# Kernel optimization log

Hardware: AMD Instinct MI355X
Metric: run time of the kernel (lower is better)

The kernel has to match this reference:

```python
import jax, jax.numpy as jnp
import numpy as np

B, S, D, H = 2, 2048, 1024, 16
HD = D // H


def setup_inputs() -> dict:
    key = jax.random.key(0)
    ks = jax.random.split(key, 12)
    s = 1.0 / np.sqrt(D)
    inp = {
        "queries": jax.random.normal(ks[0], (B, S, D), jnp.float32),
        "keys": jax.random.normal(ks[1], (B, S, D), jnp.float32),
        "values": jax.random.normal(ks[2], (B, S, D), jnp.float32),
        # True = masked out (causal upper triangle)
        "attn_mask": jnp.triu(jnp.ones((S, S), bool), k=1),
        "W_q": jax.random.normal(ks[3], (D, D), jnp.float32) * s,
        "b_q": jnp.zeros((D,), jnp.float32),
        "W_k": jax.random.normal(ks[4], (D, D), jnp.float32) * s,
        "b_k": jnp.zeros((D,), jnp.float32),
        "W_v": jax.random.normal(ks[5], (D, D), jnp.float32) * s,
        "b_v": jnp.zeros((D,), jnp.float32),
        "W_o": jax.random.normal(ks[6], (D, D), jnp.float32) * s,
        "b_o": jnp.zeros((D,), jnp.float32),
    }
    return inp


def _split_heads(x):
    b, s, _ = x.shape
    return x.reshape(b, s, H, HD).transpose(0, 2, 1, 3)  # (B,H,S,HD)


def reference(queries, keys, values, attn_mask, W_q, b_q, W_k, b_k, W_v, b_v, W_o, b_o):
    Q = _split_heads(queries @ W_q + b_q)
    K = _split_heads(keys @ W_k + b_k)
    V = _split_heads(values @ W_v + b_v)
    scale = 1.0 / np.sqrt(HD)
    scores = jnp.einsum("bhqd,bhkd->bhqk", Q, K) * scale  # (B,H,S,S)
    scores = jnp.where(attn_mask, jnp.float32(-1e9), scores)
    probs = jax.nn.softmax(scores, axis=-1)
    ctx = jnp.einsum("bhqk,bhkd->bhqd", probs, V)
    ctx = ctx.transpose(0, 2, 1, 3).reshape(queries.shape[0], queries.shape[1], D)
    return ctx @ W_o + b_o
```

## Files before the change

### kernel.cpp

```cpp
#include <hip/hip_runtime.h>
#include <hip/hip_bf16.h>
#include <math.h>

typedef __bf16 bf16x8 __attribute__((ext_vector_type(8)));
typedef float f32x4 __attribute__((ext_vector_type(4)));
typedef unsigned short u16x8 __attribute__((ext_vector_type(8)));
typedef unsigned short u16x4 __attribute__((ext_vector_type(4)));

static __device__ __forceinline__ unsigned short f2bf(float f) {
    union { float f; unsigned u; } v; v.f = f;
    unsigned r = v.u + 0x7fffu + ((v.u >> 16) & 1u);
    return (unsigned short)(r >> 16);
}

static __device__ __forceinline__ float exp2fast(float x) {
    return __builtin_exp2f(x);
}

static __device__ __forceinline__ void gload16(const void* g, void* l) {
    __builtin_amdgcn_global_load_lds((const __attribute__((address_space(1))) unsigned int*)g,
                                     (__attribute__((address_space(3))) unsigned int*)l, 16, 0, 0);
}

#define MFMA16(a, b, c) __builtin_amdgcn_mfma_f32_16x16x32_bf16((a), (b), (c), 0, 0, 0)

static __device__ __forceinline__ bf16x8 frag_swz(const unsigned short* base, int row, int chunk) {
    return *(const bf16x8*)((const char*)base + row * 128 + (((chunk ^ row) & 7) << 4));
}

struct PrepArgs {
    const float* act[3]; unsigned short* actout[3];
    const float* W[4];   unsigned short* Wt[4];
};

__global__ void prep_kernel(PrepArgs a) {
    __shared__ __align__(16) unsigned short Ws[64][66];
    const int b = blockIdx.x, t = threadIdx.x;
    if (b < 6144) {
        const int sel = b >> 11;
        const size_t i = (((size_t)(b & 2047)) * 256 + t) * 8;
        const float* in = a.act[sel];
        f32x4 v0 = *(const f32x4*)(in + i);
        f32x4 v1 = *(const f32x4*)(in + i + 4);
        u16x8 o;
#pragma unroll
        for (int j = 0; j < 4; ++j) { o[j] = f2bf(v0[j]); o[j + 4] = f2bf(v1[j]); }
        *(u16x8*)(a.actout[sel] + i) = o;
        return;
    }
    const int idx = b - 6144;
    const int z = idx >> 8;
    const int rem = idx & 255;
    const int c0 = (rem & 15) * 64;
    const int r0 = (rem >> 4) * 64;
    const float* W = a.W[z];
    unsigned short* Wt = a.Wt[z];
#pragma unroll
    for (int p = 0; p < 4; ++p) {
        int lin = p * 256 + t;
        int r = lin >> 4, cc = (lin & 15) * 4;
        f32x4 v = *(const f32x4*)(W + (size_t)(r0 + r) * 1024 + c0 + cc);
#pragma unroll
        for (int j = 0; j < 4; ++j) Ws[r][cc + j] = f2bf(v[j]);
    }
    __syncthreads();
#pragma unroll
    for (int p = 0; p < 2; ++p) {
        int lin = p * 256 + t;
        int n = lin >> 3, kc = (lin & 7) * 8;
        u16x8 o;
#pragma unroll
        for (int j = 0; j < 8; ++j) o[j] = Ws[kc + j][n];
        *(u16x8*)(Wt + (size_t)(c0 + n) * 1024 + r0 + kc) = o;
    }
}

struct QkvArgs {
    const unsigned short* A[3];
    const unsigned short* Wt[3];
    const float* bias[3];
    unsigned short* out[3];
    float scale[3];
};

__global__ __launch_bounds__(256, 3)
void gemm_qkv(QkvArgs p)
{
    __shared__ __align__(16) unsigned short As[128 * 64];
    __shared__ __align__(16) unsigned short Bs[128 * 64];

    const int z = blockIdx.z;
    const unsigned short* A  = p.A[z];
    const unsigned short* Bt = p.Wt[z];
    const float* bias = p.bias[z];
    unsigned short* out = p.out[z];
    const float oscale = p.scale[z];

    const int t = threadIdx.x, lane = t & 63, w = t >> 6;
    const int lr = lane & 15, lh = lane >> 4;
    const int m0 = blockIdx.y * 128, n0 = blockIdx.x * 128;
    const int wm = (w >> 1) * 64, wn = (w & 1) * 64;
    const int wbase = (t & 0xC0) * 8;

    f32x4 acc[4][4];
#pragma unroll
    for (int i = 0; i < 4; ++i)
#pragma unroll
        for (int j = 0; j < 4; ++j)
#pragma unroll
            for (int e = 0; e < 4; ++e) acc[i][j][e] = 0.0f;

    for (int kt = 0; kt < 16; ++kt) {
        const int k0 = kt << 6;
        __syncthreads();
#pragma unroll
        for (int q = 0; q < 4; ++q) {
            int lin = q * 256 + t;
            int row = lin >> 3, sc = (lin ^ (lin >> 3)) & 7;
            gload16(A + (size_t)(m0 + row) * 1024 + k0 + sc * 8, &As[q * 2048 + wbase]);
        }
#pragma unroll
        for (int q = 0; q < 4; ++q) {
            int lin = q * 256 + t;
            int row = lin >> 3, sc = (lin ^ (lin >> 3)) & 7;
            gload16(Bt + (size_t)(n0 + row) * 1024 + k0 + sc * 8, &Bs[q * 2048 + wbase]);
        }
        __syncthreads();
#pragma unroll
        for (int kb = 0; kb < 2; ++kb) {
            bf16x8 a[4], b[4];
#pragma unroll
            for (int i = 0; i < 4; ++i) a[i] = frag_swz(As, wm + i * 16 + lr, kb * 4 + lh);
#pragma unroll
            for (int j = 0; j < 4; ++j) b[j] = frag_swz(Bs, wn + j * 16 + lr, kb * 4 + lh);
#pragma unroll
            for (int i = 0; i < 4; ++i)
#pragma unroll
                for (int j = 0; j < 4; ++j)
                    acc[i][j] = MFMA16(a[i], b[j], acc[i][j]);
        }
    }

#pragma unroll
    for (int i = 0; i < 4; ++i) {
#pragma unroll
        for (int j = 0; j < 4; ++j) {
            const int gcol = n0 + wn + j * 16 + lr;
            const float bv = bias[gcol];
            const int h_ = gcol >> 6, hd_ = gcol & 63;
            if (z == 2) {
                const int grow0 = m0 + wm + i * 16 + lh * 4;
                const int b_ = grow0 >> 11, s_ = grow0 & 2047;
                u16x4 pk;
#pragma unroll
                for (int r = 0; r < 4; ++r) pk[r] = f2bf((acc[i][j][r] + bv) * oscale);
                *(u16x4*)(out + (((size_t)((b_ * 16 + h_) * 64 + hd_)) << 11) + s_) = pk;
            } else {
#pragma unroll
                for (int r = 0; r < 4; ++r) {
                    const int grow = m0 + wm + i * 16 + lh * 4 + r;
                    const int b_ = grow >> 11, s_ = grow & 2047;
                    out[((size_t)((b_ * 16 + h_) * 2048 + s_) << 6) + hd_] =
                        f2bf((acc[i][j][r] + bv) * oscale);
                }
            }
        }
    }
}

__global__ __launch_bounds__(256, 3)
void gemm_o_half(const unsigned short* __restrict__ A, const unsigned short* __restrict__ Bt,
                 const float* __restrict__ bias, float* __restrict__ P0, float* __restrict__ P1)
{
    __shared__ __align__(16) unsigned short As[128 * 64];
    __shared__ __align__(16) unsigned short Bs[128 * 64];

    const int z = blockIdx.z;
    float* Part = z ? P1 : P0;
    const int t = threadIdx.x, lane = t & 63, w = t >> 6;
    const int lr = lane & 15, lh = lane >> 4;
    const int m0 = blockIdx.y * 128, n0 = blockIdx.x * 128;
    const int wm = (w >> 1) * 64, wn = (w & 1) * 64;
    const int wbase = (t & 0xC0) * 8;
    const int kbase = z << 9;

    f32x4 acc[4][4];
#pragma unroll
    for (int i = 0; i < 4; ++i)
#pragma unroll
        for (int j = 0; j < 4; ++j)
#pragma unroll
            for (int e = 0; e < 4; ++e) acc[i][j][e] = 0.0f;

    for (int kt = 0; kt < 8; ++kt) {
        const int k0 = kbase + (kt << 6);
        __syncthreads();
#pragma unroll
        for (int q = 0; q < 4; ++q) {
            int lin = q * 256 + t;
            int row = lin >> 3, sc = (lin ^ (lin >> 3)) & 7;
            gload16(A + (size_t)(m0 + row) * 1024 + k0 + sc * 8, &As[q * 2048 + wbase]);
        }
#pragma unroll
        for (int q = 0; q < 4; ++q) {
            int lin = q * 256 + t;
            int row = lin >> 3, sc = (lin ^ (lin >> 3)) & 7;
            gload16(Bt + (size_t)(n0 + row) * 1024 + k0 + sc * 8, &Bs[q * 2048 + wbase]);
        }
        __syncthreads();
#pragma unroll
        for (int kb = 0; kb < 2; ++kb) {
            bf16x8 a[4], b[4];
#pragma unroll
            for (int i = 0; i < 4; ++i) a[i] = frag_swz(As, wm + i * 16 + lr, kb * 4 + lh);
#pragma unroll
            for (int j = 0; j < 4; ++j) b[j] = frag_swz(Bs, wn + j * 16 + lr, kb * 4 + lh);
#pragma unroll
            for (int i = 0; i < 4; ++i)
#pragma unroll
                for (int j = 0; j < 4; ++j)
                    acc[i][j] = MFMA16(a[i], b[j], acc[i][j]);
        }
    }

#pragma unroll
    for (int i = 0; i < 4; ++i) {
#pragma unroll
        for (int j = 0; j < 4; ++j) {
            const int gcol = n0 + wn + j * 16 + lr;
            const float bv = z ? 0.0f : bias[gcol];
#pragma unroll
            for (int r = 0; r < 4; ++r) {
                const int grow = m0 + wm + i * 16 + lh * 4 + r;
                Part[(size_t)grow * 1024 + gcol] = acc[i][j][r] + bv;
            }
        }
    }
}

__global__ void add2_kernel(const float* __restrict__ P0, const float* __restrict__ P1,
                            float* __restrict__ out) {
    const size_t i = ((size_t)blockIdx.x * 256 + threadIdx.x) * 8;
    f32x4 a0 = *(const f32x4*)(P0 + i),     a1 = *(const f32x4*)(P0 + i + 4);
    f32x4 b0 = *(const f32x4*)(P1 + i),     b1 = *(const f32x4*)(P1 + i + 4);
#pragma unroll
    for (int j = 0; j < 4; ++j) { a0[j] += b0[j]; a1[j] += b1[j]; }
    *(f32x4*)(out + i) = a0;
    *(f32x4*)(out + i + 4) = a1;
}

__global__ __launch_bounds__(512, 4)
void attn_kernel(const unsigned short* __restrict__ Qp,
                 const unsigned short* __restrict__ Kp,
                 const unsigned short* __restrict__ Vtp,
                 unsigned short* __restrict__ Cp)
{
    __shared__ __align__(16) unsigned short Ks[2][64 * 64];
    __shared__ __align__(16) unsigned short Vs[2][64 * 64];
    __shared__ __align__(16) unsigned short Pl[8][16 * 64];

    const int t = threadIdx.x, lane = t & 63, w = t >> 6;
    const int lr = lane & 15, lh = lane >> 4;
    const int wbase = (t & 0x1C0) * 8;

    const int g = blockIdx.x;
    const int local = g >> 3;
    const int bh = (g & 7) * 4 + (local >> 4);
    const int p = local & 15;
    const int grp = w >> 2;
    const int qt = 2 * p + grp;
    const int q0w = qt * 64 + (w & 3) * 16;
    const int ntiles = 2 * p + 2;
    const int mytiles = qt + 1;

    const size_t baseQK = (size_t)bh * (2048 * 64);
    const size_t baseV  = (size_t)bh * (64 * 2048);

    auto stageKV = [&](int buf, int kv0) {
        const int row = t >> 3;
        const int sc = (t ^ (t >> 3)) & 7;
        gload16(Kp + baseQK + (size_t)(kv0 + row) * 64 + sc * 8, &Ks[buf][wbase]);
        gload16(Vtp + baseV + (size_t)row * 2048 + kv0 + sc * 8, &Vs[buf][wbase]);
    };

    unsigned short* pl = &Pl[w][0];
    const int b_ = bh >> 4, h_ = bh & 15;

    const unsigned short* qrow = Qp + baseQK + (size_t)(q0w + lr) * 64 + lh * 8;
    const bf16x8 qf0 = *(const bf16x8*)qrow;
    const bf16x8 qf1 = *(const bf16x8*)(qrow + 32);

    f32x4 o[4]; float m[4], l[4];
#pragma unroll
    for (int i = 0; i < 4; ++i) {
#pragma unroll
        for (int e = 0; e < 4; ++e) o[i][e] = 0.0f;
        m[i] = -INFINITY; l[i] = 0.0f;
    }

    stageKV(0, 0);
    for (int tt = 0; tt < ntiles; ++tt) {
        __syncthreads();
        if (tt + 1 < ntiles) stageKV((tt + 1) & 1, (tt + 1) * 64);
        if (tt < mytiles) {
            const unsigned short* ks = Ks[tt & 1];
            const unsigned short* vs = Vs[tt & 1];

            f32x4 s[4];
            __builtin_amdgcn_s_setprio(1);
#pragma unroll
            for (int c = 0; c < 4; ++c) {
#pragma unroll
                for (int e = 0; e < 4; ++e) s[c][e] = 0.0f;
                s[c] = MFMA16(qf0, frag_swz(ks, c * 16 + lr, lh), s[c]);
                s[c] = MFMA16(qf1, frag_swz(ks, c * 16 + lr, 4 + lh), s[c]);
            }
            __builtin_amdgcn_s_setprio(0);

            const bool diag = (tt == qt);
            const int kv0 = tt * 64;
#pragma unroll
            for (int r = 0; r < 4; ++r) {
                const int row = lh * 4 + r;
                const int grow = q0w + row;
                float tv[4];
#pragma unroll
                for (int c = 0; c < 4; ++c) {
                    float x = s[c][r];
                    if (diag && (kv0 + c * 16 + lr > grow)) x = -1e30f;
                    tv[c] = x;
                }
                const float lmax = fmaxf(fmaxf(tv[0], tv[1]), fmaxf(tv[2], tv[3]));
                if (!__all(lmax <= m[r] + 11.0f)) {
                    float cm = lmax;
                    cm = fmaxf(cm, __shfl_xor(cm, 1));
                    cm = fmaxf(cm, __shfl_xor(cm, 2));
                    cm = fmaxf(cm, __shfl_xor(cm, 4));
                    cm = fmaxf(cm, __shfl_xor(cm, 8));
                    const float mn = fmaxf(m[r], cm);
                    const float al = exp2fast(m[r] - mn);
#pragma unroll
                    for (int hc = 0; hc < 4; ++hc) o[hc][r] *= al;
                    l[r] *= al;
                    m[r] = mn;
                }
                float rs = 0.0f;
#pragma unroll
                for (int c = 0; c < 4; ++c) {
                    const float pv = exp2fast(tv[c] - m[r]);
                    rs += pv;
                    *(__bf16*)((char*)pl + row * 128 +
                        ((c * 32 + lr * 2) ^ ((row & 7) << 4))) = (__bf16)pv;
                }
                l[r] += rs;
            }

            const bf16x8 pf0 = frag_swz(pl, lr, lh);
            const bf16x8 pf1 = frag_swz(pl, lr, 4 + lh);
            __builtin_amdgcn_s_setprio(1);
#pragma unroll
            for (int hc = 0; hc < 4; ++hc) {
                o[hc] = MFMA16(pf0, frag_swz(vs, hc * 16 + lr, lh), o[hc]);
                o[hc] = MFMA16(pf1, frag_swz(vs, hc * 16 + lr, 4 + lh), o[hc]);
            }
            __builtin_amdgcn_s_setprio(0);
        }
    }

#pragma unroll
    for (int r = 0; r < 4; ++r) {
        float sum = l[r];
        sum += __shfl_xor(sum, 1);
        sum += __shfl_xor(sum, 2);
        sum += __shfl_xor(sum, 4);
        sum += __shfl_xor(sum, 8);
        const float inv = 1.0f / sum;
        const int srow = q0w + lh * 4 + r;
#pragma unroll
        for (int hc = 0; hc < 4; ++hc) {
            Cp[(size_t)(b_ * 2048 + srow) * 1024 + h_ * 64 + hc * 16 + lr] =
                f2bf(o[hc][r] * inv);
        }
    }
}

extern "C" void kernel_launch(void* const* d_in, const int* in_sizes, int n_in,
                              void* d_out, int out_size, void* d_ws, size_t ws_size,
                              hipStream_t stream)
{
    const float* queries = (const float*)d_in[0];
    const float* keys    = (const float*)d_in[1];
    const float* values  = (const float*)d_in[2];
    const float* W_q = (const float*)d_in[4];
    const float* b_q = (const float*)d_in[5];
    const float* W_k = (const float*)d_in[6];
    const float* b_k = (const float*)d_in[7];
    const float* W_v = (const float*)d_in[8];
    const float* b_v = (const float*)d_in[9];
    const float* W_o = (const float*)d_in[10];
    const float* b_o = (const float*)d_in[11];

    constexpr size_t NE = (size_t)4 * 1024 * 1024;
    constexpr size_t WE = (size_t)1024 * 1024;
    unsigned short* qc  = (unsigned short*)d_ws;
    unsigned short* kc  = qc + NE;
    unsigned short* vc  = kc + NE;
    unsigned short* wqT = vc + NE;
    unsigned short* wkT = wqT + WE;
    unsigned short* wvT = wkT + WE;
    unsigned short* woT = wvT + WE;
    unsigned short* Qb  = woT + WE;
    unsigned short* Kb  = Qb + NE;
    unsigned short* Vtb = Kb + NE;
    unsigned short* Cb  = Vtb + NE;
    float* P0 = (float*)qc;
    float* P1 = (float*)Qb;

    const float qscale = 0.125f * 1.44269504f;

    PrepArgs pa;
    pa.act[0] = queries; pa.act[1] = keys; pa.act[2] = values;
    pa.actout[0] = qc; pa.actout[1] = kc; pa.actout[2] = vc;
    pa.W[0] = W_q; pa.W[1] = W_k; pa.W[2] = W_v; pa.W[3] = W_o;
    pa.Wt[0] = wqT; pa.Wt[1] = wkT; pa.Wt[2] = wvT; pa.Wt[3] = woT;
    prep_kernel<<<7168, 256, 0, stream>>>(pa);

    QkvArgs qp;
    qp.A[0] = qc;  qp.Wt[0] = wqT; qp.bias[0] = b_q; qp.out[0] = Qb;  qp.scale[0] = qscale;
    qp.A[1] = kc;  qp.Wt[1] = wkT; qp.bias[1] = b_k; qp.out[1] = Kb;  qp.scale[1] = 1.0f;
    qp.A[2] = vc;  qp.Wt[2] = wvT; qp.bias[2] = b_v; qp.out[2] = Vtb; qp.scale[2] = 1.0f;
    gemm_qkv<<<dim3(8, 32, 3), 256, 0, stream>>>(qp);

    attn_kernel<<<512, 512, 0, stream>>>(Qb, Kb, Vtb, Cb);

    gemm_o_half<<<dim3(8, 32, 2), 256, 0, stream>>>(Cb, woT, b_o, P0, P1);
    add2_kernel<<<2048, 256, 0, stream>>>(P0, P1, (float*)d_out);
}
```

Baseline: 293.9 us.

## Restructure causal attention blocks to process paired query tiles sequentially

Each attention block now has 4 waves and handles two 64-row query tiles in turn (qA and 31-qA), instead of 8 waves covering two adjacent tiles at once, some of which sat idle on tiles past their diagonal. The diagonal mask is compile-time specialized so only the last tile pays for the masking compare, and the setprio hints are removed. This evens out causal work across blocks and removes idle waves. In exchange each block does twice as many serial KV passes with fewer waves to hide latency, and the launch bounds and occupancy change.

```diff
diff --git a/kernel.cpp b/kernel.cpp
--- a/kernel.cpp
+++ b/kernel.cpp
@@ -6,6 +6,9 @@
 typedef float f32x4 __attribute__((ext_vector_type(4)));
 typedef unsigned short u16x8 __attribute__((ext_vector_type(8)));
 typedef unsigned short u16x4 __attribute__((ext_vector_type(4)));
+
+struct FalseC { static constexpr bool v = false; };
+struct TrueC  { static constexpr bool v = true;  };
 
 static __device__ __forceinline__ unsigned short f2bf(float f) {
     union { float f; unsigned u; } v; v.f = f;
@@ -249,7 +252,7 @@
     *(f32x4*)(out + i + 4) = a1;
 }
 
-__global__ __launch_bounds__(512, 4)
+__global__ __launch_bounds__(256, 2)
 void attn_kernel(const unsigned short* __restrict__ Qp,
                  const unsigned short* __restrict__ Kp,
                  const unsigned short* __restrict__ Vtp,
@@ -257,57 +260,55 @@
 {
     __shared__ __align__(16) unsigned short Ks[2][64 * 64];
     __shared__ __align__(16) unsigned short Vs[2][64 * 64];
-    __shared__ __align__(16) unsigned short Pl[8][16 * 64];
+    __shared__ __align__(16) unsigned short Pl[4][16 * 64];
 
     const int t = threadIdx.x, lane = t & 63, w = t >> 6;
     const int lr = lane & 15, lh = lane >> 4;
-    const int wbase = (t & 0x1C0) * 8;
+    const int wbase = (t & 0xC0) * 8;
 
     const int g = blockIdx.x;
     const int local = g >> 3;
     const int bh = (g & 7) * 4 + (local >> 4);
-    const int p = local & 15;
-    const int grp = w >> 2;
-    const int qt = 2 * p + grp;
-    const int q0w = qt * 64 + (w & 3) * 16;
-    const int ntiles = 2 * p + 2;
-    const int mytiles = qt + 1;
-
+    const int qA = local & 15;
     const size_t baseQK = (size_t)bh * (2048 * 64);
     const size_t baseV  = (size_t)bh * (64 * 2048);
 
     auto stageKV = [&](int buf, int kv0) {
-        const int row = t >> 3;
-        const int sc = (t ^ (t >> 3)) & 7;
-        gload16(Kp + baseQK + (size_t)(kv0 + row) * 64 + sc * 8, &Ks[buf][wbase]);
-        gload16(Vtp + baseV + (size_t)row * 2048 + kv0 + sc * 8, &Vs[buf][wbase]);
+#pragma unroll
+        for (int q = 0; q < 2; ++q) {
+            int lin = q * 256 + t;
+            int row = lin >> 3, sc = (lin ^ (lin >> 3)) & 7;
+            gload16(Kp + baseQK + (size_t)(kv0 + row) * 64 + sc * 8, &Ks[buf][q * 2048 + wbase]);
+        }
+#pragma unroll
+        for (int q = 0; q < 2; ++q) {
+            int lin = q * 256 + t;
+            int row = lin >> 3, sc = (lin ^ (lin >> 3)) & 7;
+            gload16(Vtp + baseV + (size_t)row * 2048 + kv0 + sc * 8, &Vs[buf][q * 2048 + wbase]);
+        }
     };
 
     unsigned short* pl = &Pl[w][0];
     const int b_ = bh >> 4, h_ = bh & 15;
 
-    const unsigned short* qrow = Qp + baseQK + (size_t)(q0w + lr) * 64 + lh * 8;
-    const bf16x8 qf0 = *(const bf16x8*)qrow;
-    const bf16x8 qf1 = *(const bf16x8*)(qrow + 32);
-
-    f32x4 o[4]; float m[4], l[4];
-#pragma unroll
-    for (int i = 0; i < 4; ++i) {
-#pragma unroll
-        for (int e = 0; e < 4; ++e) o[i][e] = 0.0f;
-        m[i] = -INFINITY; l[i] = 0.0f;
-    }
-
-    stageKV(0, 0);
-    for (int tt = 0; tt < ntiles; ++tt) {
-        __syncthreads();
-        if (tt + 1 < ntiles) stageKV((tt + 1) & 1, (tt + 1) * 64);
-        if (tt < mytiles) {
-            const unsigned short* ks = Ks[tt & 1];
-            const unsigned short* vs = Vs[tt & 1];
-
+    for (int qi = 0; qi < 2; ++qi) {
+        const int qt = qi ? (31 - qA) : qA;
+        const int q0w = qt * 64 + w * 16;
+
+        const unsigned short* qrow = Qp + baseQK + (size_t)(q0w + lr) * 64 + lh * 8;
+        const bf16x8 qf0 = *(const bf16x8*)qrow;
+        const bf16x8 qf1 = *(const bf16x8*)(qrow + 32);
+
+        f32x4 o[4]; float m[4], l[4];
+#pragma unroll
+        for (int i = 0; i < 4; ++i) {
+#pragma unroll
+            for (int e = 0; e < 4; ++e) o[i][e] = 0.0f;
+            m[i] = -INFINITY; l[i] = 0.0f;
+        }
+
+        auto tile_body = [&](auto dc, const unsigned short* ks, const unsigned short* vs) {
             f32x4 s[4];
-            __builtin_amdgcn_s_setprio(1);
 #pragma unroll
             for (int c = 0; c < 4; ++c) {
 #pragma unroll
@@ -315,19 +316,16 @@
                 s[c] = MFMA16(qf0, frag_swz(ks, c * 16 + lr, lh), s[c]);
                 s[c] = MFMA16(qf1, frag_swz(ks, c * 16 + lr, 4 + lh), s[c]);
             }
-            __builtin_amdgcn_s_setprio(0);
-
-            const bool diag = (tt == qt);
-            const int kv0 = tt * 64;
 #pragma unroll
             for (int r = 0; r < 4; ++r) {
                 const int row = lh * 4 + r;
-                const int grow = q0w + row;
                 float tv[4];
 #pragma unroll
                 for (int c = 0; c < 4; ++c) {
                     float x = s[c][r];
-                    if (diag && (kv0 + c * 16 + lr > grow)) x = -1e30f;
+                    if constexpr (decltype(dc)::v) {
+                        if (c * 16 + lr > (w * 16 + row)) x = -1e30f;
+                    }
                     tv[c] = x;
                 }
                 const float lmax = fmaxf(fmaxf(tv[0], tv[1]), fmaxf(tv[2], tv[3]));
@@ -354,32 +352,39 @@
                 }
                 l[r] += rs;
             }
-
             const bf16x8 pf0 = frag_swz(pl, lr, lh);
             const bf16x8 pf1 = frag_swz(pl, lr, 4 + lh);
-            __builtin_amdgcn_s_setprio(1);
 #pragma unroll
             for (int hc = 0; hc < 4; ++hc) {
                 o[hc] = MFMA16(pf0, frag_swz(vs, hc * 16 + lr, lh), o[hc]);
                 o[hc] = MFMA16(pf1, frag_swz(vs, hc * 16 + lr, 4 + lh), o[hc]);
             }
-            __builtin_amdgcn_s_setprio(0);
-        }
-    }
-
-#pragma unroll
-    for (int r = 0; r < 4; ++r) {
-        float sum = l[r];
-        sum += __shfl_xor(sum, 1);
-        sum += __shfl_xor(sum, 2);
-        sum += __shfl_xor(sum, 4);
-        sum += __shfl_xor(sum, 8);
-        const float inv = 1.0f / sum;
-        const int srow = q0w + lh * 4 + r;
-#pragma unroll
-        for (int hc = 0; hc < 4; ++hc) {
-            Cp[(size_t)(b_ * 2048 + srow) * 1024 + h_ * 64 + hc * 16 + lr] =
-                f2bf(o[hc][r] * inv);
+        };
+
+        __syncthreads();
+        stageKV(0, 0);
+        for (int tt = 0; tt < qt; ++tt) {
+            __syncthreads();
+            stageKV((tt + 1) & 1, (tt + 1) * 64);
+            tile_body(FalseC{}, Ks[tt & 1], Vs[tt & 1]);
+        }
+        __syncthreads();
+        tile_body(TrueC{}, Ks[qt & 1], Vs[qt & 1]);
+
+#pragma unroll
+        for (int r = 0; r < 4; ++r) {
+            float sum = l[r];
+            sum += __shfl_xor(sum, 1);
+            sum += __shfl_xor(sum, 2);
+            sum += __shfl_xor(sum, 4);
+            sum += __shfl_xor(sum, 8);
+            const float inv = 1.0f / sum;
+            const int srow = q0w + lh * 4 + r;
+#pragma unroll
+            for (int hc = 0; hc < 4; ++hc) {
+                Cp[(size_t)(b_ * 2048 + srow) * 1024 + h_ * 64 + hc * 16 + lr] =
+                    f2bf(o[hc][r] * inv);
+            }
         }
     }
 }
@@ -431,7 +436,7 @@
     qp.A[2] = vc;  qp.Wt[2] = wvT; qp.bias[2] = b_v; qp.out[2] = Vtb; qp.scale[2] = 1.0f;
     gemm_qkv<<<dim3(8, 32, 3), 256, 0, stream>>>(qp);
 
-    attn_kernel<<<512, 512, 0, stream>>>(Qb, Kb, Vtb, Cb);
+    attn_kernel<<<512, 256, 0, stream>>>(Qb, Kb, Vtb, Cb);
 
     gemm_o_half<<<dim3(8, 32, 2), 256, 0, stream>>>(Cb, woT, b_o, P0, P1);
     add2_kernel<<<2048, 256, 0, stream>>>(P0, P1, (float*)d_out);
```

Result: faster. 244.7 us (-16.7%).
